# Optimization experiments

Hardware: AMD Instinct MI355X
Metric: run time of the kernel (lower is better)

## Reference

```python
import jax, jax.numpy as jnp
import numpy as np

C = 64      # n_feats
DG = 8      # deformable groups
K = 3       # kernel size


def _lrelu(v):
    return jnp.where(v >= 0, v, 0.1 * v)


def _conv3x3(v, w, b):
    out = jax.lax.conv_general_dilated(
        v, w, window_strides=(1, 1), padding=((1, 1), (1, 1)),
        dimension_numbers=('NCHW', 'OIHW', 'NCHW'))
    return out + b[None, :, None, None]


def _up2(v):
    # bilinear upsample x2, align_corners=True (separable gather + lerp)
    B, Cc, H, W = v.shape
    def coords(n):
        c = jnp.arange(2 * n, dtype=jnp.float32) * ((n - 1) / (2 * n - 1))
        i0 = jnp.floor(c).astype(jnp.int32)
        i1 = jnp.minimum(i0 + 1, n - 1)
        f = (c - i0).astype(v.dtype)
        return i0, i1, f
    y0, y1, fy = coords(H)
    x0, x1, fx = coords(W)
    t = v[:, :, y0, :] * (1 - fy)[None, None, :, None] + v[:, :, y1, :] * fy[None, None, :, None]
    return t[:, :, :, x0] * (1 - fx)[None, None, None, :] + t[:, :, :, x1] * fx[None, None, None, :]


def _deform_conv(x, offset, mask, w, b):
    # modulated deformable conv (DCNv2), stride=1, pad=1, dil=1
    B, Cc, H, W = x.shape
    K2 = K * K
    cpg = Cc // DG
    off_y = offset[:, :DG * K2].reshape(B, DG, K2, H, W)
    off_x = offset[:, DG * K2:].reshape(B, DG, K2, H, W)
    m = mask.reshape(B, DG, 1, K2, H, W)
    ky, kx = jnp.meshgrid(jnp.arange(K) - 1, jnp.arange(K) - 1, indexing='ij')
    ky = ky.reshape(K2).astype(x.dtype)
    kx = kx.reshape(K2).astype(x.dtype)
    # absolute sampling positions [B, DG, K2, H, W]
    py = off_y + ky[None, None, :, None, None] + jnp.arange(H, dtype=x.dtype)[None, None, None, :, None]
    px = off_x + kx[None, None, :, None, None] + jnp.arange(W, dtype=x.dtype)[None, None, None, None, :]
    y0f = jnp.floor(py)
    x0f = jnp.floor(px)
    wy = py - y0f
    wx = px - x0f
    y0 = y0f.astype(jnp.int32)
    x0 = x0f.astype(jnp.int32)
    xg = x.reshape(B, DG, cpg, H * W)
    def corner(yi, xi, wgt):
        valid = ((yi >= 0) & (yi < H) & (xi >= 0) & (xi < W)).astype(x.dtype)
        yc = jnp.clip(yi, 0, H - 1)
        xc = jnp.clip(xi, 0, W - 1)
        idx = (yc * W + xc).reshape(B, DG, 1, K2 * H * W)
        g = jnp.take_along_axis(xg, jnp.broadcast_to(idx, (B, DG, cpg, K2 * H * W)), axis=3)
        g = g.reshape(B, DG, cpg, K2, H, W)
        return g * (wgt * valid)[:, :, None]
    val = (corner(y0, x0, (1 - wy) * (1 - wx))
           + corner(y0, x0 + 1, (1 - wy) * wx)
           + corner(y0 + 1, x0, wy * (1 - wx))
           + corner(y0 + 1, x0 + 1, wy * wx))
    val = val * m
    wr = w.reshape(Cc, DG, cpg, K2)
    return jnp.einsum('bgckhw,ogck->bohw', val, wr) + b[None, :, None, None]


def setup_inputs() -> dict:
    key = jax.random.key(0)
    ks = jax.random.split(key, 18)
    B, H, W = 2, 128, 128
    def p(k, shape):
        return jax.random.normal(k, shape, jnp.float32) * 0.05
    return {
        'x': jax.random.normal(ks[0], (B, C, H, W), jnp.float32),
        'y': jax.random.normal(ks[1], (B, C, H, W), jnp.float32),
        'prev_offset': jax.random.normal(ks[2], (B, C, H // 2, W // 2), jnp.float32),
        'prev_stage_fea': jax.random.normal(ks[3], (B, C, H // 2, W // 2), jnp.float32),
        'w1': p(ks[4], (C, 2 * C, 3, 3)), 'b1': jnp.zeros((C,), jnp.float32),
        'w2': p(ks[5], (C, 2 * C, 3, 3)), 'b2': jnp.zeros((C,), jnp.float32),
        'w3': p(ks[6], (C, C, 3, 3)), 'b3': jnp.zeros((C,), jnp.float32),
        'w_off': p(ks[7], (DG * 3 * K * K, C, 3, 3)), 'b_off': jnp.zeros((DG * 3 * K * K,), jnp.float32),
        'w_dcn': p(ks[8], (C, C, 3, 3)), 'b_dcn': jnp.zeros((C,), jnp.float32),
        'w_fea': p(ks[9], (C, 2 * C, 3, 3)), 'b_fea': jnp.zeros((C,), jnp.float32),
    }


def reference(x, y, prev_offset, prev_stage_fea,
              w1, b1, w2, b2, w3, b3, w_off, b_off, w_dcn, b_dcn, w_fea, b_fea):
    prev_offset = _up2(prev_offset)
    off = _lrelu(_conv3x3(jnp.concatenate([x, y], axis=1), w1, b1))
    off = _lrelu(_conv3x3(jnp.concatenate([off, prev_offset * 2], axis=1), w2, b2))
    off = _lrelu(_conv3x3(off, w3, b3))
    # DCNv2Pack: offsets/mask predicted from the offset feature
    co = _conv3x3(off, w_off, b_off)
    o1, o2, m = jnp.split(co, 3, axis=1)
    dcn_offset = jnp.concatenate([o1, o2], axis=1)
    m = jax.nn.sigmoid(m)
    fea = _deform_conv(x, dcn_offset, m, w_dcn, b_dcn)
    prev_fea = _up2(prev_stage_fea)
    out = _lrelu(_conv3x3(jnp.concatenate([fea, prev_fea], axis=1), w_fea, b_fea))
    return (off, out)
```

## Files before the change

### kernel.cpp

```cpp
#include <hip/hip_runtime.h>
#include <math.h>

typedef __bf16 bf16x8 __attribute__((ext_vector_type(8)));
typedef float f32x4 __attribute__((ext_vector_type(4)));
typedef unsigned short u16;
typedef __attribute__((address_space(3))) unsigned int lds_u32;
typedef const __attribute__((address_space(1))) unsigned int glb_u32;

__device__ __forceinline__ u16 f2bf(float f) {
    unsigned int u = __builtin_bit_cast(unsigned int, f);
    unsigned int r = (u + 0x7FFFu + ((u >> 16) & 1u)) >> 16;
    return (u16)r;
}
__device__ __forceinline__ float bf2f(u16 u) {
    unsigned int v = ((unsigned int)u) << 16;
    return __builtin_bit_cast(float, v);
}
__device__ __forceinline__ unsigned int pack2(float a, float b) {
    return (unsigned int)f2bf(a) | ((unsigned int)f2bf(b) << 16);
}
__device__ __forceinline__ bf16x8 ld8(const u16* p) {
    uint4 u = *reinterpret_cast<const uint4*>(p);
    return __builtin_bit_cast(bf16x8, u);
}
__device__ __forceinline__ void gload_lds16(const u16* g, u16* l) {
#if __has_builtin(__builtin_amdgcn_global_load_lds)
    __builtin_amdgcn_global_load_lds((glb_u32*)g, (lds_u32*)l, 16, 0, 0);
#else
    *reinterpret_cast<uint4*>(l) = *reinterpret_cast<const uint4*>(g);
#endif
}

__device__ __forceinline__ void dev_zero(u16* base, int nimg, int C, int B, int tid) {
    int idx = B * 256 + tid;
    int c8 = C >> 3;
    int tot = nimg * 516 * c8;
    if (idx >= tot) return;
    int cb = idx % c8;
    int t = idx / c8;
    int pb = t % 516;
    int img = t / 516;
    int y, x;
    if (pb < 130)      { y = 0;        x = pb; }
    else if (pb < 260) { y = 129;      x = pb - 130; }
    else if (pb < 388) { y = pb - 259; x = 0; }
    else               { y = pb - 387; x = 129; }
    u16* d = base + ((size_t)img * 16900 + (size_t)y * 130 + x) * C + cb * 8;
    uint4 z = {0u, 0u, 0u, 0u};
    *reinterpret_cast<uint4*>(d) = z;
}

__device__ __forceinline__ void dev_repack(const float* w, u16* dst,
                                           int Cout, int Cin, int mode, int B, int tid) {
    int idx = B * 256 + tid;
    int total = Cout * Cin * 9;
    if (idx >= total) return;
    int kk = idx % 9;
    int t = idx / 9;
    int ci = t % Cin;
    int o = t / Cin;
    u16 v = f2bf(w[idx]);
    size_t d;
    if (mode == 0) d = (size_t)o * (9 * Cin) + kk * Cin + ci;
    else           d = (size_t)o * 576 + (ci >> 3) * 72 + kk * 8 + (ci & 7);
    dst[d] = v;
}

__device__ __forceinline__ void dev_to_nhwc(const float* src, u16* dst,
                                            int c0, int Ctot, int B, int tid) {
    int idx = B * 256 + tid;
    int pix = idx & 16383, b = idx >> 14;
    int y = pix >> 7, x = pix & 127;
    const float* s = src + (size_t)b * 64 * 16384 + pix;
    u16* d = dst + (((size_t)b * 16900) + (size_t)(y + 1) * 130 + (x + 1)) * Ctot + c0;
#pragma unroll
    for (int q = 0; q < 8; ++q) {
        float v0 = s[(size_t)(q * 8 + 0) * 16384], v1 = s[(size_t)(q * 8 + 1) * 16384];
        float v2 = s[(size_t)(q * 8 + 2) * 16384], v3 = s[(size_t)(q * 8 + 3) * 16384];
        float v4 = s[(size_t)(q * 8 + 4) * 16384], v5 = s[(size_t)(q * 8 + 5) * 16384];
        float v6 = s[(size_t)(q * 8 + 6) * 16384], v7 = s[(size_t)(q * 8 + 7) * 16384];
        uint4 u;
        u.x = pack2(v0, v1); u.y = pack2(v2, v3); u.z = pack2(v4, v5); u.w = pack2(v6, v7);
        *reinterpret_cast<uint4*>(d + q * 8) = u;
    }
}

__device__ __forceinline__ void dev_up2(const float* src, u16* dst,
                                        int c0, int Ctot, float scale, int B, int tid) {
    int idx = B * 256 + tid;
    int pix = idx & 16383, b = idx >> 14;
    int y = pix >> 7, x = pix & 127;
    const float f = 63.0f / 127.0f;
    float cy = y * f, cx = x * f;
    float y0f = floorf(cy), x0f = floorf(cx);
    int y0 = (int)y0f, x0 = (int)x0f;
    int y1 = min(y0 + 1, 63), x1 = min(x0 + 1, 63);
    float fy = cy - y0f, fx = cx - x0f;
    float w00 = (1.f - fy) * (1.f - fx) * scale, w01 = (1.f - fy) * fx * scale;
    float w10 = fy * (1.f - fx) * scale, w11 = fy * fx * scale;
    int i00 = y0 * 64 + x0, i01 = y0 * 64 + x1, i10 = y1 * 64 + x0, i11 = y1 * 64 + x1;
    const float* s = src + (size_t)b * 64 * 4096;
    u16* d = dst + (((size_t)b * 16900) + (size_t)(y + 1) * 130 + (x + 1)) * Ctot + c0;
#pragma unroll
    for (int q = 0; q < 8; ++q) {
        float v[8];
#pragma unroll
        for (int c = 0; c < 8; ++c) {
            const float* p = s + (size_t)(q * 8 + c) * 4096;
            v[c] = w00 * p[i00] + w01 * p[i01] + w10 * p[i10] + w11 * p[i11];
        }
        uint4 u;
        u.x = pack2(v[0], v[1]); u.y = pack2(v[2], v[3]);
        u.z = pack2(v[4], v[5]); u.w = pack2(v[6], v[7]);
        *reinterpret_cast<uint4*>(d + q * 8) = u;
    }
}

__global__ __launch_bounds__(256) void preproc(
    const float* __restrict__ x, const float* __restrict__ y,
    const float* __restrict__ prev_off, const float* __restrict__ prev_fea,
    const float* __restrict__ w1, const float* __restrict__ w2,
    const float* __restrict__ w3, const float* __restrict__ w_off,
    const float* __restrict__ w_dcn, const float* __restrict__ w_fea,
    u16* __restrict__ T1, u16* __restrict__ T3, u16* __restrict__ T9,
    u16* __restrict__ T4,
    u16* __restrict__ wq1, u16* __restrict__ wq2, u16* __restrict__ wq3,
    u16* __restrict__ wqo, u16* __restrict__ wqd, u16* __restrict__ wqf) {
    int B = blockIdx.x, tid = threadIdx.x;
    if (B < 129) { dev_zero(T1, 4, 128, B, tid); return; }  B -= 129;
    if (B < 65)  { dev_zero(T9, 2, 128, B, tid); return; }  B -= 65;
    if (B < 65)  { dev_zero(T4, 4, 64, B, tid); return; }   B -= 65;
    if (B < 288) { dev_repack(w1, wq1, 64, 128, 0, B, tid); return; }   B -= 288;
    if (B < 288) { dev_repack(w2, wq2, 64, 128, 0, B, tid); return; }   B -= 288;
    if (B < 144) { dev_repack(w3, wq3, 64, 64, 0, B, tid); return; }    B -= 144;
    if (B < 486) { dev_repack(w_off, wqo, 216, 64, 0, B, tid); return; } B -= 486;
    if (B < 144) { dev_repack(w_dcn, wqd, 64, 64, 1, B, tid); return; } B -= 144;
    if (B < 288) { dev_repack(w_fea, wqf, 64, 128, 0, B, tid); return; } B -= 288;
    if (B < 128) { dev_to_nhwc(x, T1, 0, 128, B, tid); return; }        B -= 128;
    if (B < 128) { dev_to_nhwc(y, T1, 64, 128, B, tid); return; }       B -= 128;
    if (B < 128) { dev_up2(prev_off, T3, 64, 128, 2.0f, B, tid); return; } B -= 128;
    dev_up2(prev_fea, T9, 64, 128, 1.0f, B, tid);
}

template<int CIN, int WAVES, int ACTM, bool NHWC_OUT, bool OUT_PAD, int NCHW_MODE>
__global__ __launch_bounds__(WAVES * 64) void conv_tile(
    const u16* __restrict__ in, const u16* __restrict__ wgt,
    const float* __restrict__ bias,
    u16* __restrict__ outN, int c0, int Ctot,
    void* __restrict__ outC, int Cout) {
    constexpr int T = WAVES * 64;
    constexpr int MSK = (CIN == 128) ? 15 : 7;
    constexpr int RSH = (CIN == 128) ? 8 : 7;
    __shared__ __align__(16) u16 As[2][64 * CIN];

    const int tid = threadIdx.x;
    const int lane = tid & 63;
    const int wv = tid >> 6;
    const int gx = blockIdx.x;
    const int xq = gx & 3;
    const int y = (gx >> 2) & 127;
    const int b = gx >> 9;
    const int mblk = blockIdx.y << 6;
    const int n0 = lane & 15;
    const int kq = lane >> 4;
    const int cw = (CIN == 128) ? wv : (wv & 1);

    const u16* inB = in + (size_t)b * 16900 * CIN;

#define STAGE(ss, bf) {                                                        \
        _Pragma("unroll")                                                      \
        for (int i_ = 0; i_ < 4; ++i_) {                                       \
            int L_ = (i_ * T + tid) * 16;                                      \
            int row_ = L_ >> RSH;                                              \
            int c16_ = (L_ >> 4) & MSK;                                        \
            int sc_ = c16_ ^ (row_ & MSK);                                     \
            const u16* src_ = wgt + (size_t)(mblk + row_) * (9 * CIN)          \
                              + (ss) * CIN + sc_ * 8;                          \
            gload_lds16(src_, &As[bf][L_ >> 1]);                               \
        }                                                                      \
    }

    f32x4 acc[4][2] = {};

    STAGE(0, 0)
    __syncthreads();

    for (int s = 0; s < 9; ++s) {
        const int buf = s & 1;
        if (s < 8) STAGE(s + 1, buf ^ 1)

        const int dy = s / 3, dx = s - dy * 3;
        const u16* bp = inB + ((size_t)(y + dy) * 130 + (xq * 32 + n0 + dx)) * CIN
                        + cw * 32 + kq * 8;
        bf16x8 b0 = ld8(bp);
        bf16x8 b1 = ld8(bp + 16 * CIN);

        const u16* ab = &As[buf][0];
        const int colb = ((cw * 4 + kq) ^ (n0 & MSK)) * 8;
        bf16x8 a0 = ld8(ab + (0 * 16 + n0) * CIN + colb);
        bf16x8 a1 = ld8(ab + (1 * 16 + n0) * CIN + colb);
        bf16x8 a2 = ld8(ab + (2 * 16 + n0) * CIN + colb);
        bf16x8 a3 = ld8(ab + (3 * 16 + n0) * CIN + colb);

        acc[0][0] = __builtin_amdgcn_mfma_f32_16x16x32_bf16(a0, b0, acc[0][0], 0, 0, 0);
        acc[0][1] = __builtin_amdgcn_mfma_f32_16x16x32_bf16(a0, b1, acc[0][1], 0, 0, 0);
        acc[1][0] = __builtin_amdgcn_mfma_f32_16x16x32_bf16(a1, b0, acc[1][0], 0, 0, 0);
        acc[1][1] = __builtin_amdgcn_mfma_f32_16x16x32_bf16(a1, b1, acc[1][1], 0, 0, 0);
        acc[2][0] = __builtin_amdgcn_mfma_f32_16x16x32_bf16(a2, b0, acc[2][0], 0, 0, 0);
        acc[2][1] = __builtin_amdgcn_mfma_f32_16x16x32_bf16(a2, b1, acc[2][1], 0, 0, 0);
        acc[3][0] = __builtin_amdgcn_mfma_f32_16x16x32_bf16(a3, b0, acc[3][0], 0, 0, 0);
        acc[3][1] = __builtin_amdgcn_mfma_f32_16x16x32_bf16(a3, b1, acc[3][1], 0, 0, 0);

        __syncthreads();
    }
#undef STAGE

    float* red = (float*)(&As[0][0]);
#pragma unroll
    for (int mt = 0; mt < 4; ++mt)
#pragma unroll
        for (int nt = 0; nt < 2; ++nt)
            *reinterpret_cast<f32x4*>(
                &red[((wv * 8) + mt * 2 + nt) * 256 + lane * 4]) = acc[mt][nt];
    __syncthreads();

    constexpr int MTW = 4 / WAVES;
#pragma unroll
    for (int mi = 0; mi < MTW; ++mi) {
        const int mt = wv * MTW + mi;
        const int mbase = mblk + mt * 16 + kq * 4;
        float bs0 = 0.f, bs1 = 0.f, bs2 = 0.f, bs3 = 0.f;
        if (mbase < Cout) {
            bs0 = bias[mbase]; bs1 = bias[mbase + 1];
            bs2 = bias[mbase + 2]; bs3 = bias[mbase + 3];
        }
#pragma unroll
        for (int nt = 0; nt < 2; ++nt) {
            f32x4 v = {};
#pragma unroll
            for (int w2 = 0; w2 < WAVES; ++w2)
                v += *reinterpret_cast<const f32x4*>(
                    &red[((w2 * 8) + mt * 2 + nt) * 256 + lane * 4]);
            const int xx = xq * 32 + nt * 16 + n0;
            float v0 = v[0] + bs0, v1 = v[1] + bs1, v2 = v[2] + bs2, v3 = v[3] + bs3;
            if (ACTM == 1) {
                v0 = (v0 >= 0.f) ? v0 : 0.1f * v0;
                v1 = (v1 >= 0.f) ? v1 : 0.1f * v1;
                v2 = (v2 >= 0.f) ? v2 : 0.1f * v2;
                v3 = (v3 >= 0.f) ? v3 : 0.1f * v3;
            } else if (ACTM == 2) {
                if (mbase >= 144) {
                    v0 = 1.f / (1.f + expf(-v0));
                    v1 = 1.f / (1.f + expf(-v1));
                    v2 = 1.f / (1.f + expf(-v2));
                    v3 = 1.f / (1.f + expf(-v3));
                }
            }
            if (NHWC_OUT && mbase < Cout) {
                size_t pix = OUT_PAD ? ((size_t)(y + 1) * 130 + xx + 1)
                                     : ((size_t)y * 128 + xx);
                size_t off = ((size_t)b * (OUT_PAD ? 16900 : 16384) + pix) * Ctot + c0 + mbase;
                uint2 u;
                u.x = pack2(v0, v1); u.y = pack2(v2, v3);
                *reinterpret_cast<uint2*>(outN + off) = u;
            }
            if (NCHW_MODE == 1 && mbase < Cout) {
                float* oc = (float*)outC;
                size_t o = ((size_t)(b * Cout + mbase)) * 16384 + (size_t)y * 128 + xx;
                oc[o] = v0; oc[o + 16384] = v1;
                oc[o + 2 * 16384] = v2; oc[o + 3 * 16384] = v3;
            }
            if (NCHW_MODE == 2 && mbase < Cout) {
                u16* oc = (u16*)outC;
                size_t o = ((size_t)(b * Cout + mbase)) * 16384 + (size_t)y * 128 + xx;
                oc[o] = f2bf(v0); oc[o + 16384] = f2bf(v1);
                oc[o + 2 * 16384] = f2bf(v2); oc[o + 3 * 16384] = f2bf(v3);
            }
        }
    }
}

__global__ __launch_bounds__(256, 2) void dcn_fused(
    const u16* __restrict__ xn, const u16* __restrict__ co,
    const u16* __restrict__ wgt, const float* __restrict__ bias,
    u16* __restrict__ outN) {
    __shared__ u16 lw[64 * 584];
    {
        int t = threadIdx.x;
        int o = t >> 2, chunk = t & 3;
        const u16* src = wgt + o * 576 + chunk * 144;
        u16* dst = lw + o * 584 + chunk * 144;
#pragma unroll
        for (int i = 0; i < 18; ++i)
            *reinterpret_cast<uint4*>(dst + i * 8) =
                *reinterpret_cast<const uint4*>(src + i * 8);
    }
    __syncthreads();

    const int lane = threadIdx.x & 63;
    const int wv = threadIdx.x >> 6;
    const int half = blockIdx.x & 1;
    const int y = (blockIdx.x >> 1) & 127;
    const int b = blockIdx.x >> 8;
    const int n0 = lane & 15;
    const int kq = lane >> 4;
    const int xx = half * 64 + wv * 16 + n0;
    const int p = y * 128 + xx;

    const u16* cob = co + (size_t)b * 216 * 16384 + p;
    const u16* xb = xn + (size_t)b * 16900 * 128;

    float offy[18], offx[18], mvv[18];
#pragma unroll
    for (int cs = 0; cs < 18; ++cs) {
        int gk8 = cs * 4 + kq;
        offy[cs] = bf2f(cob[(size_t)gk8 * 16384]);
        offx[cs] = bf2f(cob[(size_t)(72 + gk8) * 16384]);
        mvv[cs]  = bf2f(cob[(size_t)(144 + gk8) * 16384]);
    }

    f32x4 acc[4] = {};
    float w00[2], w01[2], w10[2], w11[2];
    uint4 q00[2], q01[2], q10[2], q11[2];

#define DCN_GL(cs, st) {                                                       \
        int gk8_ = (cs) * 4 + kq;                                              \
        int g_ = (gk8_ * 57) >> 9;                                             \
        int kk_ = gk8_ - 9 * g_;                                               \
        int ky_ = (kk_ * 11) >> 5;                                             \
        int kx_ = kk_ - 3 * ky_;                                               \
        float py_ = offy[cs] + (float)(ky_ - 1) + (float)y;                    \
        float px_ = offx[cs] + (float)(kx_ - 1) + (float)xx;                   \
        float y0f_ = floorf(py_), x0f_ = floorf(px_);                          \
        float wy_ = py_ - y0f_, wx_ = px_ - x0f_;                              \
        int y0_ = (int)y0f_, x0_ = (int)x0f_, y1_ = y0_ + 1, x1_ = x0_ + 1;    \
        float m00_ = ((unsigned)y0_ < 128u && (unsigned)x0_ < 128u) ? 1.f : 0.f; \
        float m01_ = ((unsigned)y0_ < 128u && (unsigned)x1_ < 128u) ? 1.f : 0.f; \
        float m10_ = ((unsigned)y1_ < 128u && (unsigned)x0_ < 128u) ? 1.f : 0.f; \
        float m11_ = ((unsigned)y1_ < 128u && (unsigned)x1_ < 128u) ? 1.f : 0.f; \
        float mv_ = mvv[cs];                                                   \
        w00[st] = (1.f - wy_) * (1.f - wx_) * m00_ * mv_;                      \
        w01[st] = (1.f - wy_) * wx_ * m01_ * mv_;                              \
        w10[st] = wy_ * (1.f - wx_) * m10_ * mv_;                              \
        w11[st] = wy_ * wx_ * m11_ * mv_;                                      \
        int y0c_ = min(max(y0_, 0), 127), y1c_ = min(max(y1_, 0), 127);        \
        int x0c_ = min(max(x0_, 0), 127), x1c_ = min(max(x1_, 0), 127);        \
        const u16* xg_ = xb + g_ * 8;                                          \
        q00[st] = *reinterpret_cast<const uint4*>(xg_ + ((size_t)(y0c_ + 1) * 130 + x0c_ + 1) * 128); \
        q01[st] = *reinterpret_cast<const uint4*>(xg_ + ((size_t)(y0c_ + 1) * 130 + x1c_ + 1) * 128); \
        q10[st] = *reinterpret_cast<const uint4*>(xg_ + ((size_t)(y1c_ + 1) * 130 + x0c_ + 1) * 128); \
        q11[st] = *reinterpret_cast<const uint4*>(xg_ + ((size_t)(y1c_ + 1) * 130 + x1c_ + 1) * 128); \
    }

#define DCN_GU(cs, st) {                                                       \
        const unsigned int* a00_ = &q00[st].x; const unsigned int* a01_ = &q01[st].x; \
        const unsigned int* a10_ = &q10[st].x; const unsigned int* a11_ = &q11[st].x; \
        float r_[8];                                                           \
        _Pragma("unroll")                                                      \
        for (int c = 0; c < 8; ++c) {                                          \
            unsigned int u00_ = a00_[c >> 1], u01_ = a01_[c >> 1];             \
            unsigned int u10_ = a10_[c >> 1], u11_ = a11_[c >> 1];             \
            int sh_ = (c & 1) * 16;                                            \
            float f00_ = bf2f((u16)(u00_ >> sh_)), f01_ = bf2f((u16)(u01_ >> sh_)); \
            float f10_ = bf2f((u16)(u10_ >> sh_)), f11_ = bf2f((u16)(u11_ >> sh_)); \
            r_[c] = w00[st] * f00_ + w01[st] * f01_ + w10[st] * f10_ + w11[st] * f11_; \
        }                                                                      \
        uint4 bu_;                                                             \
        bu_.x = pack2(r_[0], r_[1]); bu_.y = pack2(r_[2], r_[3]);              \
        bu_.z = pack2(r_[4], r_[5]); bu_.w = pack2(r_[6], r_[7]);              \
        bf16x8 bfrag_ = __builtin_bit_cast(bf16x8, bu_);                       \
        const int kcol_ = (cs) * 32 + kq * 8;                                  \
        bf16x8 a0_ = ld8(lw + (size_t)(0 * 16 + n0) * 584 + kcol_);            \
        bf16x8 a1_ = ld8(lw + (size_t)(1 * 16 + n0) * 584 + kcol_);            \
        bf16x8 a2_ = ld8(lw + (size_t)(2 * 16 + n0) * 584 + kcol_);            \
        bf16x8 a3_ = ld8(lw + (size_t)(3 * 16 + n0) * 584 + kcol_);            \
        acc[0] = __builtin_amdgcn_mfma_f32_16x16x32_bf16(a0_, bfrag_, acc[0], 0, 0, 0); \
        acc[1] = __builtin_amdgcn_mfma_f32_16x16x32_bf16(a1_, bfrag_, acc[1], 0, 0, 0); \
        acc[2] = __builtin_amdgcn_mfma_f32_16x16x32_bf16(a2_, bfrag_, acc[2], 0, 0, 0); \
        acc[3] = __builtin_amdgcn_mfma_f32_16x16x32_bf16(a3_, bfrag_, acc[3], 0, 0, 0); \
    }

    DCN_GL(0, 0)
    DCN_GL(1, 1)
#pragma unroll
    for (int cs = 0; cs < 18; cs += 2) {
        DCN_GU(cs, 0)
        if (cs + 2 < 18) DCN_GL(cs + 2, 0)
        DCN_GU(cs + 1, 1)
        if (cs + 3 < 18) DCN_GL(cs + 3, 1)
    }
#undef DCN_GL
#undef DCN_GU

#pragma unroll
    for (int mt = 0; mt < 4; ++mt) {
        const int mbase = mt * 16 + kq * 4;
        float v0 = acc[mt][0] + bias[mbase];
        float v1 = acc[mt][1] + bias[mbase + 1];
        float v2 = acc[mt][2] + bias[mbase + 2];
        float v3 = acc[mt][3] + bias[mbase + 3];
        size_t off = ((size_t)b * 16900 + (size_t)(y + 1) * 130 + (xx + 1)) * 128 + mbase;
        uint2 u;
        u.x = pack2(v0, v1); u.y = pack2(v2, v3);
        *reinterpret_cast<uint2*>(outN + off) = u;
    }
}

#define T1_OFF 0u
#define T3_OFF 8652800u
#define T9_OFF 17305600u
#define T4_OFF 25958400u
#define T5_OFF 30284800u
#define T6_OFF 34611200u
#define W1_OFF 48766976u
#define W2_OFF 48914432u
#define W3_OFF 49061888u
#define WF_OFF 49135616u
#define WO_OFF 49283072u
#define WD_OFF 49577984u

extern "C" void kernel_launch(void* const* d_in, const int* in_sizes, int n_in,
                              void* d_out, int out_size, void* d_ws, size_t ws_size,
                              hipStream_t stream) {
    const float* x        = (const float*)d_in[0];
    const float* y        = (const float*)d_in[1];
    const float* prev_off = (const float*)d_in[2];
    const float* prev_fea = (const float*)d_in[3];
    const float* w1 = (const float*)d_in[4];  const float* b1 = (const float*)d_in[5];
    const float* w2 = (const float*)d_in[6];  const float* b2 = (const float*)d_in[7];
    const float* w3 = (const float*)d_in[8];  const float* b3 = (const float*)d_in[9];
    const float* w_off = (const float*)d_in[10]; const float* b_off = (const float*)d_in[11];
    const float* w_dcn = (const float*)d_in[12]; const float* b_dcn = (const float*)d_in[13];
    const float* w_fea = (const float*)d_in[14]; const float* b_fea = (const float*)d_in[15];

    float* out_off = (float*)d_out;
    float* out_out = (float*)d_out + (size_t)2 * 64 * 16384;

    char* ws = (char*)d_ws;
    u16* T1 = (u16*)(ws + T1_OFF);
    u16* T3 = (u16*)(ws + T3_OFF);
    u16* T9 = (u16*)(ws + T9_OFF);
    u16* T4 = (u16*)(ws + T4_OFF);
    u16* T5 = (u16*)(ws + T5_OFF);
    u16* T6 = (u16*)(ws + T6_OFF);
    u16* wq1 = (u16*)(ws + W1_OFF);
    u16* wq2 = (u16*)(ws + W2_OFF);
    u16* wq3 = (u16*)(ws + W3_OFF);
    u16* wqf = (u16*)(ws + WF_OFF);
    u16* wqo = (u16*)(ws + WO_OFF);
    u16* wqd = (u16*)(ws + WD_OFF);

    preproc<<<dim3(2409), dim3(256), 0, stream>>>(
        x, y, prev_off, prev_fea, w1, w2, w3, w_off, w_dcn, w_fea,
        T1, T3, T9, T4, wq1, wq2, wq3, wqo, wqd, wqf);

    conv_tile<128, 4, 1, true, true, 0><<<dim3(1024, 1), dim3(256), 0, stream>>>(
        T1, wq1, b1, T3, 0, 128, nullptr, 64);
    conv_tile<128, 4, 1, true, true, 0><<<dim3(1024, 1), dim3(256), 0, stream>>>(
        T3, wq2, b2, T4, 0, 64, nullptr, 64);
    conv_tile<64, 2, 1, true, true, 1><<<dim3(1024, 1), dim3(128), 0, stream>>>(
        T4, wq3, b3, T5, 0, 64, out_off, 64);
    conv_tile<64, 2, 2, false, false, 2><<<dim3(1024, 4), dim3(128), 0, stream>>>(
        T5, wqo, b_off, nullptr, 0, 0, T6, 216);
    dcn_fused<<<dim3(512), dim3(256), 0, stream>>>(T1, T6, wqd, b_dcn, T9);
    conv_tile<128, 4, 1, false, false, 1><<<dim3(1024, 1), dim3(256), 0, stream>>>(
        T9, wqf, b_fea, nullptr, 0, 0, out_out, 64);
}
```

Measured before the change: 143.7 us.

## Widen conv tiles to 64 pixels and cut cross-wave K-split reduction

Each conv block now covers 64 output pixels per row instead of 32. Waves are split into pixel columns and a smaller K-split (2 for CIN=128, none for CIN=64), and the grid is halved to match. Each staged weight tile in LDS is now reused by twice as many pixels, and the LDS reduction is dropped (CIN=64) or reduced to a single add from one slice. In exchange there are fewer blocks per launch, which may lower occupancy and latency hiding.

```diff
diff --git a/kernel.cpp b/kernel.cpp
--- a/kernel.cpp
+++ b/kernel.cpp
@@ -142,13 +142,17 @@
     dev_up2(prev_fea, T9, 64, 128, 1.0f, B, tid);
 }
 
-template<int CIN, int WAVES, int ACTM, bool NHWC_OUT, bool OUT_PAD, int NCHW_MODE>
+template<int CIN, int WAVES, int KSPLIT, int ACTM, bool NHWC_OUT, bool OUT_PAD, int NCHW_MODE>
 __global__ __launch_bounds__(WAVES * 64) void conv_tile(
     const u16* __restrict__ in, const u16* __restrict__ wgt,
     const float* __restrict__ bias,
     u16* __restrict__ outN, int c0, int Ctot,
     void* __restrict__ outC, int Cout) {
     constexpr int T = WAVES * 64;
+    constexpr int PXW = WAVES / KSPLIT;
+    constexpr int BPR = 4 / PXW;
+    constexpr int KCH = CIN / KSPLIT;
+    constexpr int CSTEPS = KCH / 32;
     constexpr int MSK = (CIN == 128) ? 15 : 7;
     constexpr int RSH = (CIN == 128) ? 8 : 7;
     __shared__ __align__(16) u16 As[2][64 * CIN];
@@ -156,20 +160,22 @@
     const int tid = threadIdx.x;
     const int lane = tid & 63;
     const int wv = tid >> 6;
+    const int kslice = wv % KSPLIT;
+    const int pxc = wv / KSPLIT;
     const int gx = blockIdx.x;
-    const int xq = gx & 3;
-    const int y = (gx >> 2) & 127;
-    const int b = gx >> 9;
+    const int xh = gx % BPR;
+    const int y = (gx / BPR) & 127;
+    const int b = gx / (BPR * 128);
     const int mblk = blockIdx.y << 6;
     const int n0 = lane & 15;
     const int kq = lane >> 4;
-    const int cw = (CIN == 128) ? wv : (wv & 1);
+    const int xbase = xh * (PXW * 32) + pxc * 32;
 
     const u16* inB = in + (size_t)b * 16900 * CIN;
 
 #define STAGE(ss, bf) {                                                        \
         _Pragma("unroll")                                                      \
-        for (int i_ = 0; i_ < 4; ++i_) {                                       \
+        for (int i_ = 0; i_ < (8 * CIN) / T; ++i_) {                           \
             int L_ = (i_ * T + tid) * 16;                                      \
             int row_ = L_ >> RSH;                                              \
             int c16_ = (L_ >> 4) & MSK;                                        \
@@ -190,44 +196,54 @@
         if (s < 8) STAGE(s + 1, buf ^ 1)
 
         const int dy = s / 3, dx = s - dy * 3;
-        const u16* bp = inB + ((size_t)(y + dy) * 130 + (xq * 32 + n0 + dx)) * CIN
-                        + cw * 32 + kq * 8;
-        bf16x8 b0 = ld8(bp);
-        bf16x8 b1 = ld8(bp + 16 * CIN);
-
+        const u16* brow = inB + ((size_t)(y + dy) * 130 + (xbase + n0 + dx)) * CIN
+                          + kq * 8;
         const u16* ab = &As[buf][0];
-        const int colb = ((cw * 4 + kq) ^ (n0 & MSK)) * 8;
-        bf16x8 a0 = ld8(ab + (0 * 16 + n0) * CIN + colb);
-        bf16x8 a1 = ld8(ab + (1 * 16 + n0) * CIN + colb);
-        bf16x8 a2 = ld8(ab + (2 * 16 + n0) * CIN + colb);
-        bf16x8 a3 = ld8(ab + (3 * 16 + n0) * CIN + colb);
-
-        acc[0][0] = __builtin_amdgcn_mfma_f32_16x16x32_bf16(a0, b0, acc[0][0], 0, 0, 0);
-        acc[0][1] = __builtin_amdgcn_mfma_f32_16x16x32_bf16(a0, b1, acc[0][1], 0, 0, 0);
-        acc[1][0] = __builtin_amdgcn_mfma_f32_16x16x32_bf16(a1, b0, acc[1][0], 0, 0, 0);
-        acc[1][1] = __builtin_amdgcn_mfma_f32_16x16x32_bf16(a1, b1, acc[1][1], 0, 0, 0);
-        acc[2][0] = __builtin_amdgcn_mfma_f32_16x16x32_bf16(a2, b0, acc[2][0], 0, 0, 0);
-        acc[2][1] = __builtin_amdgcn_mfma_f32_16x16x32_bf16(a2, b1, acc[2][1], 0, 0, 0);
-        acc[3][0] = __builtin_amdgcn_mfma_f32_16x16x32_bf16(a3, b0, acc[3][0], 0, 0, 0);
-        acc[3][1] = __builtin_amdgcn_mfma_f32_16x16x32_bf16(a3, b1, acc[3][1], 0, 0, 0);
-
+#pragma unroll
+        for (int c = 0; c < CSTEPS; ++c) {
+            const int kch = kslice * KCH + c * 32;
+            bf16x8 b0 = ld8(brow + kch);
+            bf16x8 b1 = ld8(brow + 16 * CIN + kch);
+            const int colb = (((kch >> 3) + kq) ^ (n0 & MSK)) * 8;
+            bf16x8 a0 = ld8(ab + (0 * 16 + n0) * CIN + colb);
+            bf16x8 a1 = ld8(ab + (1 * 16 + n0) * CIN + colb);
+            bf16x8 a2 = ld8(ab + (2 * 16 + n0) * CIN + colb);
+            bf16x8 a3 = ld8(ab + (3 * 16 + n0) * CIN + colb);
+            acc[0][0] = __builtin_amdgcn_mfma_f32_16x16x32_bf16(a0, b0, acc[0][0], 0, 0, 0);
+            acc[0][1] = __builtin_amdgcn_mfma_f32_16x16x32_bf16(a0, b1, acc[0][1], 0, 0, 0);
+            acc[1][0] = __builtin_amdgcn_mfma_f32_16x16x32_bf16(a1, b0, acc[1][0], 0, 0, 0);
+            acc[1][1] = __builtin_amdgcn_mfma_f32_16x16x32_bf16(a1, b1, acc[1][1], 0, 0, 0);
+            acc[2][0] = __builtin_amdgcn_mfma_f32_16x16x32_bf16(a2, b0, acc[2][0], 0, 0, 0);
+            acc[2][1] = __builtin_amdgcn_mfma_f32_16x16x32_bf16(a2, b1, acc[2][1], 0, 0, 0);
+            acc[3][0] = __builtin_amdgcn_mfma_f32_16x16x32_bf16(a3, b0, acc[3][0], 0, 0, 0);
+            acc[3][1] = __builtin_amdgcn_mfma_f32_16x16x32_bf16(a3, b1, acc[3][1], 0, 0, 0);
+        }
         __syncthreads();
     }
 #undef STAGE
 
-    float* red = (float*)(&As[0][0]);
-#pragma unroll
-    for (int mt = 0; mt < 4; ++mt)
-#pragma unroll
-        for (int nt = 0; nt < 2; ++nt)
-            *reinterpret_cast<f32x4*>(
-                &red[((wv * 8) + mt * 2 + nt) * 256 + lane * 4]) = acc[mt][nt];
-    __syncthreads();
-
-    constexpr int MTW = 4 / WAVES;
-#pragma unroll
-    for (int mi = 0; mi < MTW; ++mi) {
-        const int mt = wv * MTW + mi;
+    if (KSPLIT == 2) {
+        float* red = (float*)(&As[0][0]);
+        if (kslice == 1) {
+#pragma unroll
+            for (int mt = 0; mt < 4; ++mt)
+#pragma unroll
+                for (int nt = 0; nt < 2; ++nt)
+                    *reinterpret_cast<f32x4*>(
+                        &red[((pxc * 8) + mt * 2 + nt) * 256 + lane * 4]) = acc[mt][nt];
+        }
+        __syncthreads();
+        if (kslice == 1) return;
+#pragma unroll
+        for (int mt = 0; mt < 4; ++mt)
+#pragma unroll
+            for (int nt = 0; nt < 2; ++nt)
+                acc[mt][nt] += *reinterpret_cast<const f32x4*>(
+                    &red[((pxc * 8) + mt * 2 + nt) * 256 + lane * 4]);
+    }
+
+#pragma unroll
+    for (int mt = 0; mt < 4; ++mt) {
         const int mbase = mblk + mt * 16 + kq * 4;
         float bs0 = 0.f, bs1 = 0.f, bs2 = 0.f, bs3 = 0.f;
         if (mbase < Cout) {
@@ -236,13 +252,9 @@
         }
 #pragma unroll
         for (int nt = 0; nt < 2; ++nt) {
-            f32x4 v = {};
-#pragma unroll
-            for (int w2 = 0; w2 < WAVES; ++w2)
-                v += *reinterpret_cast<const f32x4*>(
-                    &red[((w2 * 8) + mt * 2 + nt) * 256 + lane * 4]);
-            const int xx = xq * 32 + nt * 16 + n0;
-            float v0 = v[0] + bs0, v1 = v[1] + bs1, v2 = v[2] + bs2, v3 = v[3] + bs3;
+            const int xx = xbase + nt * 16 + n0;
+            float v0 = acc[mt][nt][0] + bs0, v1 = acc[mt][nt][1] + bs1;
+            float v2 = acc[mt][nt][2] + bs2, v3 = acc[mt][nt][3] + bs3;
             if (ACTM == 1) {
                 v0 = (v0 >= 0.f) ? v0 : 0.1f * v0;
                 v1 = (v1 >= 0.f) ? v1 : 0.1f * v1;
@@ -454,15 +466,15 @@
         x, y, prev_off, prev_fea, w1, w2, w3, w_off, w_dcn, w_fea,
         T1, T3, T9, T4, wq1, wq2, wq3, wqo, wqd, wqf);
 
-    conv_tile<128, 4, 1, true, true, 0><<<dim3(1024, 1), dim3(256), 0, stream>>>(
+    conv_tile<128, 4, 2, 1, true, true, 0><<<dim3(512, 1), dim3(256), 0, stream>>>(
         T1, wq1, b1, T3, 0, 128, nullptr, 64);
-    conv_tile<128, 4, 1, true, true, 0><<<dim3(1024, 1), dim3(256), 0, stream>>>(
+    conv_tile<128, 4, 2, 1, true, true, 0><<<dim3(512, 1), dim3(256), 0, stream>>>(
         T3, wq2, b2, T4, 0, 64, nullptr, 64);
-    conv_tile<64, 2, 1, true, true, 1><<<dim3(1024, 1), dim3(128), 0, stream>>>(
+    conv_tile<64, 2, 1, 1, true, true, 1><<<dim3(512, 1), dim3(128), 0, stream>>>(
         T4, wq3, b3, T5, 0, 64, out_off, 64);
-    conv_tile<64, 2, 2, false, false, 2><<<dim3(1024, 4), dim3(128), 0, stream>>>(
+    conv_tile<64, 2, 1, 2, false, false, 2><<<dim3(512, 4), dim3(128), 0, stream>>>(
         T5, wqo, b_off, nullptr, 0, 0, T6, 216);
     dcn_fused<<<dim3(512), dim3(256), 0, stream>>>(T1, T6, wqd, b_dcn, T9);
-    conv_tile<128, 4, 1, false, false, 1><<<dim3(1024, 1), dim3(256), 0, stream>>>(
+    conv_tile<128, 4, 2, 1, false, false, 1><<<dim3(512, 1), dim3(256), 0, stream>>>(
         T9, wqf, b_fea, nullptr, 0, 0, out_out, 64);
 }
```

Result: no change. 142.1 us (-1.1%).
